# Kernel tuning notes

Hardware: AMD Instinct MI355X
Metric: run time of the kernel (lower is better)

The kernel has to match this reference:

```python
import jax, jax.numpy as jnp
import numpy as np

B, N, D, H = 4, 2048, 1024, 16
HD = D // H
SCALE = D ** -0.5  # NOTE: original scales by dimension**-0.5 (not head_dim**-0.5)


def setup_inputs() -> dict:
    key = jax.random.key(0)
    k1, k2, k3 = jax.random.split(key, 3)
    x = jax.random.normal(k1, (B, N, D), dtype=jnp.float32)
    w_qkv = jax.random.normal(k2, (D, 3 * D), dtype=jnp.float32) * (D ** -0.5)
    w_proj = jax.random.normal(k3, (D, D), dtype=jnp.float32) * (D ** -0.5)
    b_proj = jnp.zeros((D,), dtype=jnp.float32)
    return {"x": x, "w_qkv": w_qkv, "w_proj": w_proj, "b_proj": b_proj}


def reference(x, w_qkv, w_proj, b_proj):
    # qkv projection: [B,N,3D] -> split into q,k,v each [B,H,N,HD]
    qkv = x @ w_qkv
    qkv = qkv.reshape(B, N, 3, H, HD).transpose(2, 0, 3, 1, 4)  # [3,B,H,N,HD]
    q, k, v = qkv[0], qkv[1], qkv[2]
    scores = jnp.einsum('bhid,bhjd->bhij', q, k) * SCALE
    attn = jax.nn.softmax(scores, axis=-1)
    out = jnp.einsum('bhij,bhjd->bhid', attn, v)  # [B,H,N,HD]
    out = out.transpose(0, 2, 1, 3).reshape(B, N, D)
    return out @ w_proj + b_proj
```

## Files before the change

kernel.cpp:

```cpp
#include <hip/hip_runtime.h>
#include <stdint.h>

#define Bdim 4
#define Nseq 2048
#define Dmod 1024
#define Hn   16
#define HD   64
#define SCALE 0.03125f
#define L2E   1.44269504089f

typedef __attribute__((ext_vector_type(8))) short short8;
typedef __attribute__((ext_vector_type(8))) unsigned short ushort8;
typedef __attribute__((ext_vector_type(4))) float f32x4;
typedef __attribute__((ext_vector_type(16))) float f32x16;

typedef __attribute__((address_space(3))) uint32_t lds_u32;
typedef __attribute__((address_space(1))) const uint32_t glob_u32;

static __device__ __forceinline__ void gload_lds16(const unsigned short* g, unsigned short* l) {
    __builtin_amdgcn_global_load_lds((glob_u32*)(const void*)g, (lds_u32*)(void*)l, 16, 0, 0);
}

static __device__ __forceinline__ unsigned short f2bf(float f) {
    union { float f; uint32_t u; } v; v.f = f;
    uint32_t r = (v.u + 0x7FFFu + ((v.u >> 16) & 1u)) >> 16;
    return (unsigned short)r;
}

__global__ __launch_bounds__(256) void cast_x_kernel(const float* __restrict__ in,
                                                     unsigned short* __restrict__ out, int n4) {
    int i = blockIdx.x * blockDim.x + threadIdx.x;
    int stride = gridDim.x * blockDim.x;
    for (; i < n4; i += stride) {
        float4 v = reinterpret_cast<const float4*>(in)[i];
        ushort4 o;
        o.x = f2bf(v.x); o.y = f2bf(v.y); o.z = f2bf(v.z); o.w = f2bf(v.w);
        reinterpret_cast<ushort4*>(out)[i] = o;
    }
}

__global__ void transpose_cast_kernel(const float* __restrict__ in,
                                      unsigned short* __restrict__ out, int R, int C) {
    __shared__ unsigned short t[32][33];
    int c0 = blockIdx.x * 32, r0 = blockIdx.y * 32;
    int tx = threadIdx.x, ty = threadIdx.y;
#pragma unroll
    for (int i = 0; i < 4; ++i)
        t[ty + i*8][tx] = f2bf(in[(size_t)(r0 + ty + i*8) * C + c0 + tx]);
    __syncthreads();
#pragma unroll
    for (int i = 0; i < 4; ++i)
        out[(size_t)(c0 + ty + i*8) * R + r0 + tx] = t[tx][ty + i*8];
}

template<bool OUT_BF16, bool BIAS>
__global__ __launch_bounds__(256) void gemm_bt_kernel(const unsigned short* __restrict__ A,
                                                      const unsigned short* __restrict__ Bt,
                                                      void* __restrict__ Cv,
                                                      const float* __restrict__ bias,
                                                      int M, int N, int K) {
    __shared__ unsigned short Al[128 * 64];
    __shared__ unsigned short Bl[128 * 64];
    int tid = threadIdx.x;
    int lane = tid & 63, wv = tid >> 6;
    int wr = (wv >> 1) * 64, wc = (wv & 1) * 64;
    int lr = lane & 15, lg = lane >> 4, lk = lg * 8;
    int m0 = blockIdx.y * 128, n0 = blockIdx.x * 128;

    int srow = wv * 8 + (lane >> 3);
    int scol = (lane & 7) * 8;
    const unsigned short* ag = A  + (size_t)(m0 + srow) * K + scol;
    const unsigned short* bg = Bt + (size_t)(n0 + srow) * K + scol;
    unsigned short* la = Al + wv * 512;
    unsigned short* lb = Bl + wv * 512;

    f32x4 acc[4][4];
#pragma unroll
    for (int i = 0; i < 4; ++i)
#pragma unroll
        for (int j = 0; j < 4; ++j) acc[i][j] = (f32x4)0.f;

    for (int k0 = 0; k0 < K; k0 += 64) {
        __syncthreads();
#pragma unroll
        for (int i = 0; i < 4; ++i) {
            gload_lds16(ag + (size_t)i * 32 * K + k0, la + i * 2048);
            gload_lds16(bg + (size_t)i * 32 * K + k0, lb + i * 2048);
        }
        __syncthreads();
#pragma unroll
        for (int ks = 0; ks < 2; ++ks) {
            short8 a[4], b[4];
#pragma unroll
            for (int mi = 0; mi < 4; ++mi)
                a[mi] = *reinterpret_cast<const short8*>(Al + (wr + mi*16 + lr) * 64 + ks*32 + lk);
#pragma unroll
            for (int nj = 0; nj < 4; ++nj)
                b[nj] = *reinterpret_cast<const short8*>(Bl + (wc + nj*16 + lr) * 64 + ks*32 + lk);
#pragma unroll
            for (int mi = 0; mi < 4; ++mi)
#pragma unroll
                for (int nj = 0; nj < 4; ++nj)
                    acc[mi][nj] = __builtin_amdgcn_mfma_f32_16x16x32_bf16(a[mi], b[nj], acc[mi][nj], 0, 0, 0);
        }
    }
#pragma unroll
    for (int mi = 0; mi < 4; ++mi) {
#pragma unroll
        for (int nj = 0; nj < 4; ++nj) {
            int r = m0 + wr + mi*16 + lg*4;
            int c = n0 + wc + nj*16 + lr;
            float bv = BIAS ? bias[c] : 0.f;
#pragma unroll
            for (int i = 0; i < 4; ++i) {
                float v = acc[mi][nj][i] + bv;
                if (OUT_BF16)
                    reinterpret_cast<unsigned short*>(Cv)[(size_t)(r + i) * N + c] = f2bf(v);
                else
                    reinterpret_cast<float*>(Cv)[(size_t)(r + i) * N + c] = v;
            }
        }
    }
}

__global__ __launch_bounds__(256) void transpose_v_kernel(const unsigned short* __restrict__ qkv,
                                                          unsigned short* __restrict__ vT) {
    __shared__ unsigned short t[64][68];
    int bh = blockIdx.y, b = bh >> 4, h = bh & 15;
    int j0 = blockIdx.x * 64;
    int tid = threadIdx.x;
#pragma unroll
    for (int p = 0; p < 4; ++p) {
        int e = p * 256 + tid;
        int jj = e >> 4;
        int d4 = (e & 15) * 4;
        const unsigned short* src = qkv + (size_t)(b*Nseq + j0 + jj) * 3072 + 2048 + h*64 + d4;
        ushort4 v = *reinterpret_cast<const ushort4*>(src);
        *reinterpret_cast<ushort4*>(&t[jj][d4]) = v;
    }
    __syncthreads();
#pragma unroll
    for (int p = 0; p < 4; ++p) {
        int e = p * 256 + tid;
        int d = e >> 4;
        int j4 = (e & 15) * 4;
        ushort4 v;
        v.x = t[j4 + 0][d]; v.y = t[j4 + 1][d]; v.z = t[j4 + 2][d]; v.w = t[j4 + 3][d];
        *reinterpret_cast<ushort4*>(vT + ((size_t)bh * 64 + d) * Nseq + j0 + j4) = v;
    }
}

__global__ __launch_bounds__(256) void attn_kernel(const unsigned short* __restrict__ qkv,
                                                   const unsigned short* __restrict__ vT,
                                                   unsigned short* __restrict__ attn_o) {
    __shared__ unsigned short Kl[64 * 64];
    __shared__ unsigned short Vl[64 * 64];
    __shared__ unsigned short Pl[4 * 32 * 64];

    int w = blockIdx.x;
    int lid = (w & 7) * 128 + (w >> 3);
    int bh = lid >> 4, qb = lid & 15;
    int b = bh >> 4, h = bh & 15;

    int tid = threadIdx.x, lane = tid & 63, wv = tid >> 6;
    int lr = lane & 31, hi = lane >> 5;
    int q0 = qb * 128 + wv * 32;

    short8 qf[4];
    {
        const unsigned short* qrow = qkv + (size_t)(b * Nseq + q0 + lr) * 3072 + h * 64 + hi * 8;
#pragma unroll
        for (int ks = 0; ks < 4; ++ks)
            qf[ks] = *reinterpret_cast<const short8*>(qrow + ks * 16);
    }

    float mrun = -1e30f, lrun = 0.f;
    f32x16 oacc0 = (f32x16)0.f, oacc1 = (f32x16)0.f;

    int sr = tid >> 2;
    int sc = (tid & 3) * 32;
    const unsigned short* kg = qkv + (size_t)(b * Nseq + sr) * 3072 + 1024 + h * 64 + sc / 2;
    const unsigned short* vg = vT + ((size_t)(bh * 64 + sr)) * Nseq + sc / 2;
    int swz0 = sr * 128 + ((sc) ^ ((sr & 7) << 4));
    int swz1 = sr * 128 + ((sc + 16) ^ ((sr & 7) << 4));
    int rswz = (lr & 7) << 4;
    char* PlW = (char*)Pl + wv * 4096 + lr * 128;

    ushort8 k0r = *reinterpret_cast<const ushort8*>(kg);
    ushort8 k1r = *reinterpret_cast<const ushort8*>(kg + 8);
    ushort8 v0r = *reinterpret_cast<const ushort8*>(vg);
    ushort8 v1r = *reinterpret_cast<const ushort8*>(vg + 8);

    for (int jt = 0; jt < Nseq; jt += 64) {
        __syncthreads();
        *reinterpret_cast<ushort8*>((char*)Kl + swz0) = k0r;
        *reinterpret_cast<ushort8*>((char*)Kl + swz1) = k1r;
        *reinterpret_cast<ushort8*>((char*)Vl + swz0) = v0r;
        *reinterpret_cast<ushort8*>((char*)Vl + swz1) = v1r;
        int jn = jt + 64;
        if (jn < Nseq) {
            k0r = *reinterpret_cast<const ushort8*>(kg + (size_t)jn * 3072);
            k1r = *reinterpret_cast<const ushort8*>(kg + (size_t)jn * 3072 + 8);
            v0r = *reinterpret_cast<const ushort8*>(vg + jn);
            v1r = *reinterpret_cast<const ushort8*>(vg + jn + 8);
        }
        __syncthreads();

        f32x16 s0 = (f32x16)0.f, s1 = (f32x16)0.f;
        __builtin_amdgcn_s_setprio(1);
#pragma unroll
        for (int ks = 0; ks < 4; ++ks) {
            int cb = ks * 32 + hi * 16;
            short8 kf0 = *reinterpret_cast<const short8*>((char*)Kl + lr * 128 + (cb ^ rswz));
            short8 kf1 = *reinterpret_cast<const short8*>((char*)Kl + (lr + 32) * 128 + (cb ^ rswz));
            s0 = __builtin_amdgcn_mfma_f32_32x32x16_bf16(kf0, qf[ks], s0, 0, 0, 0);
            s1 = __builtin_amdgcn_mfma_f32_32x32x16_bf16(kf1, qf[ks], s1, 0, 0, 0);
        }
        __builtin_amdgcn_s_setprio(0);

        float t[16];
#pragma unroll
        for (int i = 0; i < 16; ++i) t[i] = fmaxf(s0[i], s1[i]);
#pragma unroll
        for (int st = 8; st > 0; st >>= 1)
#pragma unroll
            for (int i = 0; i < st; ++i) t[i] = fmaxf(t[i], t[i + st]);
        float mloc = fmaxf(t[0], __shfl_xor(t[0], 32));
        float mnew = fmaxf(mrun, mloc * SCALE);
        float fac = __builtin_amdgcn_exp2f((mrun - mnew) * L2E);
        const float c1 = SCALE * L2E;
        float c0 = -mnew * L2E;
        float p0[16], p1[16];
#pragma unroll
        for (int i = 0; i < 16; ++i) p0[i] = __builtin_amdgcn_exp2f(fmaf(s0[i], c1, c0));
#pragma unroll
        for (int i = 0; i < 16; ++i) p1[i] = __builtin_amdgcn_exp2f(fmaf(s1[i], c1, c0));
        float a[16];
#pragma unroll
        for (int i = 0; i < 16; ++i) a[i] = p0[i] + p1[i];
#pragma unroll
        for (int st = 8; st > 0; st >>= 1)
#pragma unroll
            for (int i = 0; i < st; ++i) a[i] = a[i] + a[i + st];
        float ps = a[0] + __shfl_xor(a[0], 32);
        lrun = lrun * fac + ps;
        mrun = mnew;
#pragma unroll
        for (int i = 0; i < 16; ++i) { oacc0[i] *= fac; oacc1[i] *= fac; }

        uint32_t W[16];
#pragma unroll
        for (int m = 0; m < 8; ++m) {
            asm("v_cvt_pk_bf16_f32 %0, %1, %2" : "=v"(W[m])   : "v"(p0[2*m]), "v"(p0[2*m+1]));
            asm("v_cvt_pk_bf16_f32 %0, %1, %2" : "=v"(W[8+m]) : "v"(p1[2*m]), "v"(p1[2*m+1]));
        }
#pragma unroll
        for (int tt = 0; tt < 8; ++tt) {
            uint64_t val = (uint64_t)W[2*tt] | ((uint64_t)W[2*tt+1] << 32);
            *reinterpret_cast<uint64_t*>(PlW + ((16*tt + 8*hi) ^ rswz)) = val;
        }

        __builtin_amdgcn_s_setprio(1);
#pragma unroll
        for (int ks4 = 0; ks4 < 4; ++ks4) {
            int cb = ks4 * 32 + hi * 16;
            short8 pf  = *reinterpret_cast<const short8*>(PlW + (cb ^ rswz));
            short8 vf0 = *reinterpret_cast<const short8*>((char*)Vl + lr * 128 + (cb ^ rswz));
            short8 vf1 = *reinterpret_cast<const short8*>((char*)Vl + (lr + 32) * 128 + (cb ^ rswz));
            oacc0 = __builtin_amdgcn_mfma_f32_32x32x16_bf16(vf0, pf, oacc0, 0, 0, 0);
            oacc1 = __builtin_amdgcn_mfma_f32_32x32x16_bf16(vf1, pf, oacc1, 0, 0, 0);
        }
        __builtin_amdgcn_s_setprio(0);
    }

    float inv = 1.f / lrun;
    unsigned short* orow = attn_o + (size_t)(b * Nseq + q0 + lr) * Dmod + h * 64;
#pragma unroll
    for (int db = 0; db < 2; ++db)
#pragma unroll
        for (int g = 0; g < 4; ++g) {
            ushort4 o4;
            float v0 = (db ? oacc1[4*g+0] : oacc0[4*g+0]) * inv;
            float v1 = (db ? oacc1[4*g+1] : oacc0[4*g+1]) * inv;
            float v2 = (db ? oacc1[4*g+2] : oacc0[4*g+2]) * inv;
            float v3 = (db ? oacc1[4*g+3] : oacc0[4*g+3]) * inv;
            o4.x = f2bf(v0); o4.y = f2bf(v1); o4.z = f2bf(v2); o4.w = f2bf(v3);
            int d = db * 32 + 8 * g + 4 * hi;
            *reinterpret_cast<ushort4*>(orow + d) = o4;
        }
}

extern "C" void kernel_launch(void* const* d_in, const int* in_sizes, int n_in,
                              void* d_out, int out_size, void* d_ws, size_t ws_size,
                              hipStream_t stream) {
    const float* x      = (const float*)d_in[0];
    const float* w_qkv  = (const float*)d_in[1];
    const float* w_proj = (const float*)d_in[2];
    const float* b_proj = (const float*)d_in[3];
    float* out = (float*)d_out;
    char* ws = (char*)d_ws;

    unsigned short* qkv    = (unsigned short*)(ws);
    unsigned short* vT     = (unsigned short*)(ws + 50331648);
    unsigned short* xb     = (unsigned short*)(ws + 67108864);
    unsigned short* attn_o = xb;
    unsigned short* wqkvT  = (unsigned short*)(ws + 83886080);
    unsigned short* wprojT = (unsigned short*)(ws + 90177536);

    cast_x_kernel<<<2048, 256, 0, stream>>>(x, xb, (Bdim*Nseq*Dmod)/4);
    transpose_cast_kernel<<<dim3(3072/32, 1024/32), dim3(32, 8), 0, stream>>>(w_qkv, wqkvT, 1024, 3072);
    transpose_cast_kernel<<<dim3(1024/32, 1024/32), dim3(32, 8), 0, stream>>>(w_proj, wprojT, 1024, 1024);
    gemm_bt_kernel<true, false><<<dim3(3072/128, 8192/128), 256, 0, stream>>>(
        xb, wqkvT, qkv, nullptr, Bdim*Nseq, 3*Dmod, Dmod);
    transpose_v_kernel<<<dim3(Nseq/64, Bdim*Hn), 256, 0, stream>>>(qkv, vT);
    attn_kernel<<<1024, 256, 0, stream>>>(qkv, vT, attn_o);
    gemm_bt_kernel<false, true><<<dim3(1024/128, 8192/128), 256, 0, stream>>>(
        attn_o, wprojT, out, b_proj, Bdim*Nseq, Dmod, Dmod);
}
```

Measured before the change: 250.9 us.

## Process 64 query rows per wave and skip softmax rescale when max stable

```diff
diff --git a/kernel.cpp b/kernel.cpp
--- a/kernel.cpp
+++ b/kernel.cpp
@@ -150,32 +150,35 @@
     }
 }
 
-__global__ __launch_bounds__(256) void attn_kernel(const unsigned short* __restrict__ qkv,
-                                                   const unsigned short* __restrict__ vT,
-                                                   unsigned short* __restrict__ attn_o) {
+__global__ __launch_bounds__(256, 2) void attn_kernel(const unsigned short* __restrict__ qkv,
+                                                      const unsigned short* __restrict__ vT,
+                                                      unsigned short* __restrict__ attn_o) {
     __shared__ unsigned short Kl[64 * 64];
     __shared__ unsigned short Vl[64 * 64];
-    __shared__ unsigned short Pl[4 * 32 * 64];
+    __shared__ unsigned short Pl[4 * 64 * 64];
 
     int w = blockIdx.x;
-    int lid = (w & 7) * 128 + (w >> 3);
-    int bh = lid >> 4, qb = lid & 15;
+    int lid = (w & 7) * 64 + (w >> 3);
+    int bh = lid >> 3, qb = lid & 7;
     int b = bh >> 4, h = bh & 15;
 
     int tid = threadIdx.x, lane = tid & 63, wv = tid >> 6;
     int lr = lane & 31, hi = lane >> 5;
-    int q0 = qb * 128 + wv * 32;
-
-    short8 qf[4];
+    int q0 = qb * 256 + wv * 64;
+
+    short8 qfA[4], qfB[4];
     {
-        const unsigned short* qrow = qkv + (size_t)(b * Nseq + q0 + lr) * 3072 + h * 64 + hi * 8;
-#pragma unroll
-        for (int ks = 0; ks < 4; ++ks)
-            qf[ks] = *reinterpret_cast<const short8*>(qrow + ks * 16);
-    }
-
-    float mrun = -1e30f, lrun = 0.f;
-    f32x16 oacc0 = (f32x16)0.f, oacc1 = (f32x16)0.f;
+        const unsigned short* qrowA = qkv + (size_t)(b * Nseq + q0 + lr) * 3072 + h * 64 + hi * 8;
+        const unsigned short* qrowB = qrowA + (size_t)32 * 3072;
+#pragma unroll
+        for (int ks = 0; ks < 4; ++ks) {
+            qfA[ks] = *reinterpret_cast<const short8*>(qrowA + ks * 16);
+            qfB[ks] = *reinterpret_cast<const short8*>(qrowB + ks * 16);
+        }
+    }
+
+    float mrunA = -1e30f, lrunA = 0.f, mrunB = -1e30f, lrunB = 0.f;
+    f32x16 oA0 = (f32x16)0.f, oA1 = (f32x16)0.f, oB0 = (f32x16)0.f, oB1 = (f32x16)0.f;
 
     int sr = tid >> 2;
     int sc = (tid & 3) * 32;
@@ -184,7 +187,7 @@
     int swz0 = sr * 128 + ((sc) ^ ((sr & 7) << 4));
     int swz1 = sr * 128 + ((sc + 16) ^ ((sr & 7) << 4));
     int rswz = (lr & 7) << 4;
-    char* PlW = (char*)Pl + wv * 4096 + lr * 128;
+    char* PlW = (char*)Pl + wv * 8192 + lr * 128;
 
     ushort8 k0r = *reinterpret_cast<const ushort8*>(kg);
     ushort8 k1r = *reinterpret_cast<const ushort8*>(kg + 8);
@@ -206,87 +209,115 @@
         }
         __syncthreads();
 
-        f32x16 s0 = (f32x16)0.f, s1 = (f32x16)0.f;
+        f32x16 sA0 = (f32x16)0.f, sA1 = (f32x16)0.f, sB0 = (f32x16)0.f, sB1 = (f32x16)0.f;
         __builtin_amdgcn_s_setprio(1);
 #pragma unroll
         for (int ks = 0; ks < 4; ++ks) {
             int cb = ks * 32 + hi * 16;
             short8 kf0 = *reinterpret_cast<const short8*>((char*)Kl + lr * 128 + (cb ^ rswz));
             short8 kf1 = *reinterpret_cast<const short8*>((char*)Kl + (lr + 32) * 128 + (cb ^ rswz));
-            s0 = __builtin_amdgcn_mfma_f32_32x32x16_bf16(kf0, qf[ks], s0, 0, 0, 0);
-            s1 = __builtin_amdgcn_mfma_f32_32x32x16_bf16(kf1, qf[ks], s1, 0, 0, 0);
+            sA0 = __builtin_amdgcn_mfma_f32_32x32x16_bf16(kf0, qfA[ks], sA0, 0, 0, 0);
+            sA1 = __builtin_amdgcn_mfma_f32_32x32x16_bf16(kf1, qfA[ks], sA1, 0, 0, 0);
+            sB0 = __builtin_amdgcn_mfma_f32_32x32x16_bf16(kf0, qfB[ks], sB0, 0, 0, 0);
+            sB1 = __builtin_amdgcn_mfma_f32_32x32x16_bf16(kf1, qfB[ks], sB1, 0, 0, 0);
         }
         __builtin_amdgcn_s_setprio(0);
 
-        float t[16];
-#pragma unroll
-        for (int i = 0; i < 16; ++i) t[i] = fmaxf(s0[i], s1[i]);
+        float tA[16], tB[16];
+#pragma unroll
+        for (int i = 0; i < 16; ++i) { tA[i] = fmaxf(sA0[i], sA1[i]); tB[i] = fmaxf(sB0[i], sB1[i]); }
 #pragma unroll
         for (int st = 8; st > 0; st >>= 1)
 #pragma unroll
-            for (int i = 0; i < st; ++i) t[i] = fmaxf(t[i], t[i + st]);
-        float mloc = fmaxf(t[0], __shfl_xor(t[0], 32));
-        float mnew = fmaxf(mrun, mloc * SCALE);
-        float fac = __builtin_amdgcn_exp2f((mrun - mnew) * L2E);
+            for (int i = 0; i < st; ++i) { tA[i] = fmaxf(tA[i], tA[i + st]); tB[i] = fmaxf(tB[i], tB[i + st]); }
+        float mlocA = fmaxf(tA[0], __shfl_xor(tA[0], 32)) * SCALE;
+        float mlocB = fmaxf(tB[0], __shfl_xor(tB[0], 32)) * SCALE;
+
+        if (!__all((mlocA <= mrunA + 8.f) && (mlocB <= mrunB + 8.f))) {
+            float mnA = fmaxf(mrunA, mlocA);
+            float fA = __builtin_amdgcn_exp2f((mrunA - mnA) * L2E);
+            float mnB = fmaxf(mrunB, mlocB);
+            float fB = __builtin_amdgcn_exp2f((mrunB - mnB) * L2E);
+            lrunA *= fA; lrunB *= fB; mrunA = mnA; mrunB = mnB;
+#pragma unroll
+            for (int i = 0; i < 16; ++i) {
+                oA0[i] *= fA; oA1[i] *= fA; oB0[i] *= fB; oB1[i] *= fB;
+            }
+        }
+
         const float c1 = SCALE * L2E;
-        float c0 = -mnew * L2E;
-        float p0[16], p1[16];
-#pragma unroll
-        for (int i = 0; i < 16; ++i) p0[i] = __builtin_amdgcn_exp2f(fmaf(s0[i], c1, c0));
-#pragma unroll
-        for (int i = 0; i < 16; ++i) p1[i] = __builtin_amdgcn_exp2f(fmaf(s1[i], c1, c0));
-        float a[16];
-#pragma unroll
-        for (int i = 0; i < 16; ++i) a[i] = p0[i] + p1[i];
+        float c0A = -mrunA * L2E, c0B = -mrunB * L2E;
+        float pA0[16], pA1[16], pB0[16], pB1[16];
+#pragma unroll
+        for (int i = 0; i < 16; ++i) {
+            pA0[i] = __builtin_amdgcn_exp2f(fmaf(sA0[i], c1, c0A));
+            pA1[i] = __builtin_amdgcn_exp2f(fmaf(sA1[i], c1, c0A));
+            pB0[i] = __builtin_amdgcn_exp2f(fmaf(sB0[i], c1, c0B));
+            pB1[i] = __builtin_amdgcn_exp2f(fmaf(sB1[i], c1, c0B));
+        }
+
+        uint32_t WA[16], WB[16];
+#pragma unroll
+        for (int m = 0; m < 8; ++m) {
+            asm("v_cvt_pk_bf16_f32 %0, %1, %2" : "=v"(WA[m])   : "v"(pA0[2*m]), "v"(pA0[2*m+1]));
+            asm("v_cvt_pk_bf16_f32 %0, %1, %2" : "=v"(WA[8+m]) : "v"(pA1[2*m]), "v"(pA1[2*m+1]));
+            asm("v_cvt_pk_bf16_f32 %0, %1, %2" : "=v"(WB[m])   : "v"(pB0[2*m]), "v"(pB0[2*m+1]));
+            asm("v_cvt_pk_bf16_f32 %0, %1, %2" : "=v"(WB[8+m]) : "v"(pB1[2*m]), "v"(pB1[2*m+1]));
+        }
+#pragma unroll
+        for (int tt = 0; tt < 8; ++tt) {
+            uint64_t valA = (uint64_t)WA[2*tt] | ((uint64_t)WA[2*tt+1] << 32);
+            uint64_t valB = (uint64_t)WB[2*tt] | ((uint64_t)WB[2*tt+1] << 32);
+            int off = (16*tt + 8*hi) ^ rswz;
+            *reinterpret_cast<uint64_t*>(PlW + off) = valA;
+            *reinterpret_cast<uint64_t*>(PlW + 4096 + off) = valB;
+        }
+
+        float aA[16], aB[16];
+#pragma unroll
+        for (int i = 0; i < 16; ++i) { aA[i] = pA0[i] + pA1[i]; aB[i] = pB0[i] + pB1[i]; }
 #pragma unroll
         for (int st = 8; st > 0; st >>= 1)
 #pragma unroll
-            for (int i = 0; i < st; ++i) a[i] = a[i] + a[i + st];
-        float ps = a[0] + __shfl_xor(a[0], 32);
-        lrun = lrun * fac + ps;
-        mrun = mnew;
-#pragma unroll
-        for (int i = 0; i < 16; ++i) { oacc0[i] *= fac; oacc1[i] *= fac; }
-
-        uint32_t W[16];
-#pragma unroll
-        for (int m = 0; m < 8; ++m) {
-            asm("v_cvt_pk_bf16_f32 %0, %1, %2" : "=v"(W[m])   : "v"(p0[2*m]), "v"(p0[2*m+1]));
-            asm("v_cvt_pk_bf16_f32 %0, %1, %2" : "=v"(W[8+m]) : "v"(p1[2*m]), "v"(p1[2*m+1]));
-        }
-#pragma unroll
-        for (int tt = 0; tt < 8; ++tt) {
-            uint64_t val = (uint64_t)W[2*tt] | ((uint64_t)W[2*tt+1] << 32);
-            *reinterpret_cast<uint64_t*>(PlW + ((16*tt + 8*hi) ^ rswz)) = val;
-        }
+            for (int i = 0; i < st; ++i) { aA[i] += aA[i + st]; aB[i] += aB[i + st]; }
+        lrunA += aA[0] + __shfl_xor(aA[0], 32);
+        lrunB += aB[0] + __shfl_xor(aB[0], 32);
 
         __builtin_amdgcn_s_setprio(1);
 #pragma unroll
         for (int ks4 = 0; ks4 < 4; ++ks4) {
             int cb = ks4 * 32 + hi * 16;
-            short8 pf  = *reinterpret_cast<const short8*>(PlW + (cb ^ rswz));
             short8 vf0 = *reinterpret_cast<const short8*>((char*)Vl + lr * 128 + (cb ^ rswz));
             short8 vf1 = *reinterpret_cast<const short8*>((char*)Vl + (lr + 32) * 128 + (cb ^ rswz));
-            oacc0 = __builtin_amdgcn_mfma_f32_32x32x16_bf16(vf0, pf, oacc0, 0, 0, 0);
-            oacc1 = __builtin_amdgcn_mfma_f32_32x32x16_bf16(vf1, pf, oacc1, 0, 0, 0);
+            short8 pfA = *reinterpret_cast<const short8*>(PlW + (cb ^ rswz));
+            short8 pfB = *reinterpret_cast<const short8*>(PlW + 4096 + (cb ^ rswz));
+            oA0 = __builtin_amdgcn_mfma_f32_32x32x16_bf16(vf0, pfA, oA0, 0, 0, 0);
+            oA1 = __builtin_amdgcn_mfma_f32_32x32x16_bf16(vf1, pfA, oA1, 0, 0, 0);
+            oB0 = __builtin_amdgcn_mfma_f32_32x32x16_bf16(vf0, pfB, oB0, 0, 0, 0);
+            oB1 = __builtin_amdgcn_mfma_f32_32x32x16_bf16(vf1, pfB, oB1, 0, 0, 0);
         }
         __builtin_amdgcn_s_setprio(0);
     }
 
-    float inv = 1.f / lrun;
-    unsigned short* orow = attn_o + (size_t)(b * Nseq + q0 + lr) * Dmod + h * 64;
+    float invA = 1.f / lrunA, invB = 1.f / lrunB;
+    unsigned short* orowA = attn_o + (size_t)(b * Nseq + q0 + lr) * Dmod + h * 64;
+    unsigned short* orowB = attn_o + (size_t)(b * Nseq + q0 + 32 + lr) * Dmod + h * 64;
 #pragma unroll
     for (int db = 0; db < 2; ++db)
 #pragma unroll
         for (int g = 0; g < 4; ++g) {
+            int d = db * 32 + 8 * g + 4 * hi;
             ushort4 o4;
-            float v0 = (db ? oacc1[4*g+0] : oacc0[4*g+0]) * inv;
-            float v1 = (db ? oacc1[4*g+1] : oacc0[4*g+1]) * inv;
-            float v2 = (db ? oacc1[4*g+2] : oacc0[4*g+2]) * inv;
-            float v3 = (db ? oacc1[4*g+3] : oacc0[4*g+3]) * inv;
-            o4.x = f2bf(v0); o4.y = f2bf(v1); o4.z = f2bf(v2); o4.w = f2bf(v3);
-            int d = db * 32 + 8 * g + 4 * hi;
-            *reinterpret_cast<ushort4*>(orow + d) = o4;
+            o4.x = f2bf((db ? oA1[4*g+0] : oA0[4*g+0]) * invA);
+            o4.y = f2bf((db ? oA1[4*g+1] : oA0[4*g+1]) * invA);
+            o4.z = f2bf((db ? oA1[4*g+2] : oA0[4*g+2]) * invA);
+            o4.w = f2bf((db ? oA1[4*g+3] : oA0[4*g+3]) * invA);
+            *reinterpret_cast<ushort4*>(orowA + d) = o4;
+            o4.x = f2bf((db ? oB1[4*g+0] : oB0[4*g+0]) * invB);
+            o4.y = f2bf((db ? oB1[4*g+1] : oB0[4*g+1]) * invB);
+            o4.z = f2bf((db ? oB1[4*g+2] : oB0[4*g+2]) * invB);
+            o4.w = f2bf((db ? oB1[4*g+3] : oB0[4*g+3]) * invB);
+            *reinterpret_cast<ushort4*>(orowB + d) = o4;
         }
 }
 
@@ -313,7 +344,7 @@
     gemm_bt_kernel<true, false><<<dim3(3072/128, 8192/128), 256, 0, stream>>>(
         xb, wqkvT, qkv, nullptr, Bdim*Nseq, 3*Dmod, Dmod);
     transpose_v_kernel<<<dim3(Nseq/64, Bdim*Hn), 256, 0, stream>>>(qkv, vT);
-    attn_kernel<<<1024, 256, 0, stream>>>(qkv, vT, attn_o);
+    attn_kernel<<<512, 256, 0, stream>>>(qkv, vT, attn_o);
     gemm_bt_kernel<false, true><<<dim3(1024/128, 8192/128), 256, 0, stream>>>(
         attn_o, wprojT, out, b_proj, Bdim*Nseq, Dmod, Dmod);
 }
```

Result: faster. 224.5 us (-10.5%).
